# Performance work log

Measured on AMD Instinct MI355X. Metric: run time of the kernel, lower is better.

## Reference

```python
import jax, jax.numpy as jnp
import numpy as np

T, WQ, WS, C, H, W = 2, 75, 25, 640, 10, 10
WAY, SHOT = 5, 5
HID = C // 16
SCALE_VALUE = 30.0
ATTEN_SCALE_VALUE = 50.0
FROM_VALUE = 0.5
VALUE_INTERVAL = 0.3
BN_EPS = 1e-5
NORM_EPS = 1e-12


def _leaky(x):
    return jnp.where(x >= 0, x, 0.2 * x)


def _l2norm(x, axis):
    n = jnp.sqrt(jnp.sum(x * x, axis=axis, keepdims=True))
    return x / jnp.maximum(n, NORM_EPS)


def _embed(x, W_conv, bn_gamma, bn_beta, bn_mean, bn_var):
    # 1x1 conv (no bias) + eval-mode BatchNorm + LeakyReLU(0.2)
    # x: [t, n, c, h, w] -> [t, n, c, h, w]
    y = jnp.einsum('oc,tnchw->tnohw', W_conv, x)
    inv = bn_gamma / jnp.sqrt(bn_var + BN_EPS)
    y = y * inv[:, None, None] + (bn_beta - bn_mean * inv)[:, None, None]
    return _leaky(y)


def setup_inputs() -> dict:
    key = jax.random.key(0)
    ks = jax.random.split(key, 5)
    return {
        'query_feat': jax.random.normal(ks[0], (T, WQ, C, H, W), dtype=jnp.float32),
        'support_feat': jax.random.normal(ks[1], (T, WS, C, H, W), dtype=jnp.float32),
        'W_conv': jax.random.normal(ks[2], (C, C), dtype=jnp.float32) * 0.02,
        'bn_gamma': jnp.ones((C,), jnp.float32),
        'bn_beta': jnp.zeros((C,), jnp.float32),
        'bn_mean': jnp.zeros((C,), jnp.float32),
        'bn_var': jnp.ones((C,), jnp.float32),
        'psi_w1': jax.random.normal(ks[3], (C, HID), dtype=jnp.float32) * 0.04,
        'psi_b1': jnp.zeros((HID,), jnp.float32),
        'psi_w2': jax.random.normal(ks[4], (HID, 1), dtype=jnp.float32) * 0.15,
        'psi_b2': jnp.zeros((1,), jnp.float32),
        'way_num': WAY,
        'shot_num': SHOT,
    }


def reference(query_feat, support_feat, W_conv, bn_gamma, bn_beta, bn_mean, bn_var,
              psi_w1, psi_b1, psi_w2, psi_b2, way_num, shot_num):
    t, wq, c, h, w = query_feat.shape
    ws = support_feat.shape[1]
    hw = h * w

    # embedded + normalized features for the gated branch
    w_query = _embed(query_feat, W_conv, bn_gamma, bn_beta, bn_mean, bn_var)
    w_query = w_query.reshape(t, wq, c, hw).transpose(0, 1, 3, 2)      # [t, wq, hw, c]
    w_support = _embed(support_feat, W_conv, bn_gamma, bn_beta, bn_mean, bn_var)
    w_support = w_support.reshape(t, ws, c, hw).transpose(0, 2, 1, 3).reshape(t, c, ws * hw)
    w_query = _l2norm(w_query, axis=3)
    w_support = _l2norm(w_support, axis=1)

    # cosine similarity of embedded features: [t, wq, hw, ws*hw]
    f_x = jnp.einsum('tqpc,tck->tqpk', w_query, w_support)

    # AEAModule: per-location adaptive threshold from f_psi MLP
    hid = _leaky(w_query @ psi_w1 + psi_b1)                            # [t, wq, hw, HID]
    clamp_value = jax.nn.sigmoid(hid @ psi_w2 + psi_b2) * VALUE_INTERVAL + FROM_VALUE
    clamp_fx = jax.nn.sigmoid(ATTEN_SCALE_VALUE * (f_x - clamp_value))
    atten_score = clamp_fx / jnp.maximum(
        jnp.sum(jnp.abs(clamp_fx), axis=-1, keepdims=True), NORM_EPS)  # L1 normalize

    # raw-feature cosine similarity
    qf = _l2norm(query_feat.reshape(t, wq, c, hw).transpose(0, 1, 3, 2), axis=3)
    sf = _l2norm(support_feat.reshape(t, ws, c, hw).transpose(0, 2, 1, 3).reshape(t, c, ws * hw), axis=1)
    match_score = jnp.einsum('tqpc,tck->tqpk', qf, sf)                 # [t, wq, hw, ws*hw]

    # gate, regroup support axis into (way, shot, hw_s), reduce
    ams = (atten_score * match_score).reshape(t, wq, hw, way_num, shot_num, hw)
    score = ams.sum(axis=-1).mean(axis=(2, 4)) * SCALE_VALUE           # [t, wq, way]
    return score
```

## Files before the change

### kernel.cpp

```cpp
#include <hip/hip_runtime.h>
#include <stdint.h>

#define T_    2
#define WQ_   75
#define WS_   25
#define C_    640
#define HW_   100
#define HID_  40
#define WAY_  5
#define QP_   (WQ_*HW_)
#define SP_   (WS_*HW_)
#define QPAD_ 128
#define KPAD_ 512
#define KROWS_ (WAY_*KPAD_)
#define C8_   (C_/8)
#define BM_   128
#define QSTR_ (C8_*QPAD_*8)

typedef _Float16 f16;
typedef _Float16 f16x8 __attribute__((ext_vector_type(8)));
typedef _Float16 f16x4 __attribute__((ext_vector_type(4)));
typedef _Float16 f16x16 __attribute__((ext_vector_type(16)));
typedef float    f32x4 __attribute__((ext_vector_type(4)));
typedef float    f32x16 __attribute__((ext_vector_type(16)));
typedef uint32_t u32;

__device__ __forceinline__ void gl_lds16(const f16* g, f16* l) {
  __builtin_amdgcn_global_load_lds(
      (const __attribute__((address_space(1))) u32*)g,
      (__attribute__((address_space(3))) u32*)l, 16, 0, 0);
}

__global__ __launch_bounds__(512) void k0_invnorm(
    const float* __restrict__ q, const float* __restrict__ s,
    float* __restrict__ rq_inv, float* __restrict__ rq_nrm,
    float* __restrict__ rs_inv, float* __restrict__ rs_nrm) {
  __shared__ float part[4][128];
  int b = blockIdx.x;
  int t = b / (WQ_ + WS_);
  int n = b % (WQ_ + WS_);
  int tid = threadIdx.x;
  int seg = tid >> 7, p = tid & 127;
  const float* base; float* oi; float* on; int idx;
  if (n < WQ_) {
    base = q + ((size_t)(t*WQ_ + n))*C_*HW_;
    idx = t*QP_ + n*HW_ + p; oi = rq_inv; on = rq_nrm;
  } else {
    int m = n - WQ_;
    base = s + ((size_t)(t*WS_ + m))*C_*HW_;
    idx = t*SP_ + m*HW_ + p; oi = rs_inv; on = rs_nrm;
  }
  float ss = 0.f;
  if (p < HW_) {
    for (int c = seg*160; c < seg*160 + 160; ++c) {
      float v = base[c*HW_ + p]; ss += v*v;
    }
  }
  part[seg][p] = ss;
  __syncthreads();
  if (seg == 0 && p < HW_) {
    float tot = part[0][p] + part[1][p] + part[2][p] + part[3][p];
    float nrm = fmaxf(sqrtf(tot), 1e-12f);
    oi[idx] = 1.f/nrm; on[idx] = nrm;
  }
}

__global__ __launch_bounds__(256) void kw_packW(
    const float* __restrict__ W, const float* __restrict__ w1,
    f16* __restrict__ Wr, f16* __restrict__ Wt8, f16* __restrict__ w1t) {
  int idx = blockIdx.x*256 + threadIdx.x;
  if (idx < C_*C8_) {
    int o = idx / C8_, c8 = idx % C8_;
    f16x8 v;
#pragma unroll
    for (int i = 0; i < 8; ++i) v[i] = (f16)W[(size_t)o*C_ + c8*8 + i];
    *reinterpret_cast<f16x8*>(Wr + (size_t)o*C_ + c8*8) = v;
    *reinterpret_cast<f16x8*>(Wt8 + ((size_t)c8*C_ + o)*8) = v;
  } else if (idx < C_*C8_ + 48*C8_) {
    int k2 = idx - C_*C8_;
    int h = k2 / C8_, c8 = k2 % C8_;
    f16x8 v;
#pragma unroll
    for (int i = 0; i < 8; ++i)
      v[i] = (h < HID_) ? (f16)w1[(size_t)(c8*8+i)*HID_ + h] : (f16)0.f;
    *reinterpret_cast<f16x8*>(w1t + (size_t)h*C_ + c8*8) = v;
  }
}

__global__ __launch_bounds__(256) void k1_pack_qraw(
    const float* __restrict__ q, const float* __restrict__ rq_inv,
    f16* __restrict__ Bq_raw) {
  int b = blockIdx.x;
  int ct = b % 10; b /= 10;
  int qq = b % WQ_; int t = b / WQ_;
  int c0 = ct*64;
  size_t tq = (size_t)t*WQ_ + qq;
  __shared__ float lds[64*HW_];
  const float4* s4 = reinterpret_cast<const float4*>(
      q + ((tq)*C_ + c0)*HW_);
  float4* l4 = reinterpret_cast<float4*>(lds);
  for (int i = threadIdx.x; i < 64*HW_/4; i += 256) l4[i] = s4[i];
  __syncthreads();
  for (int ch = threadIdx.x; ch < 8*QPAD_; ch += 256) {
    int lc8 = ch / QPAD_, p = ch % QPAD_;
    float inv = (p < HW_) ? rq_inv[t*QP_ + qq*HW_ + p] : 0.f;
    f16x8 v;
#pragma unroll
    for (int i = 0; i < 8; ++i) {
      float x = (p < HW_) ? lds[(lc8*8 + i)*HW_ + p] : 0.f;
      v[i] = (f16)(x * inv);
    }
    *reinterpret_cast<f16x8*>(Bq_raw + (tq*C8_ + c0/8 + lc8)*((size_t)QPAD_*8) + (size_t)p*8) = v;
  }
}

__global__ __launch_bounds__(256) void k2_pack_sraw(
    const float* __restrict__ s, const float* __restrict__ rs_inv,
    f16* __restrict__ As_raw) {
  int b = blockIdx.x;
  int ct = b % 10; b /= 10;
  int n = b % WS_; int t = b / WS_;
  int c0 = ct*64;
  __shared__ float lds[64*HW_];
  const float4* s4 = reinterpret_cast<const float4*>(
      s + (((size_t)(t*WS_ + n))*C_ + c0)*HW_);
  float4* l4 = reinterpret_cast<float4*>(lds);
  for (int i = threadIdx.x; i < 64*HW_/4; i += 256) l4[i] = s4[i];
  __syncthreads();
  for (int ch = threadIdx.x; ch < HW_*8; ch += 256) {
    int p = ch / 8, cc = ch % 8;
    float inv = rs_inv[t*SP_ + n*HW_ + p];
    f16x8 v;
#pragma unroll
    for (int i = 0; i < 8; ++i) v[i] = (f16)(lds[(cc*8 + i)*HW_ + p] * inv);
    int k = n*HW_ + p;
    int way = k / 500, ki = k % 500;
    size_t row = (size_t)way*KPAD_ + ki;
    *reinterpret_cast<f16x8*>(As_raw + ((size_t)(t*C8_ + c0/8 + cc)*KROWS_ + row)*8) = v;
  }
}

__global__ __launch_bounds__(512) void k3_embed_support(
    const f16* __restrict__ As_raw, const f16* __restrict__ Wt8,
    const float* __restrict__ rs_nrm,
    const float* __restrict__ g, const float* __restrict__ be,
    const float* __restrict__ mu, const float* __restrict__ va,
    f16* __restrict__ As_emb) {
  int b = blockIdx.x;
  int t = b / (KROWS_/32);
  int row0 = (b % (KROWS_/32)) * 32;
  int tid = threadIdx.x, wv = tid >> 6, lane = tid & 63;
  int mf = wv & 1, nh = wv >> 1;
  __shared__ f16 Alds[32*32];
  __shared__ f16 Blds[32*C_];
  __shared__ float rowss[32];
  f32x4 acc[10];
#pragma unroll
  for (int i = 0; i < 10; ++i) acc[i] = (f32x4){0.f,0.f,0.f,0.f};

  for (int cs = 0; cs < 20; ++cs) {
    if (tid < 128) {
      int c8l = tid >> 5, r = tid & 31;
      *reinterpret_cast<f16x8*>(Alds + (c8l*32 + r)*8) =
        *reinterpret_cast<const f16x8*>(
            As_raw + ((size_t)(t*C8_ + cs*4 + c8l)*KROWS_ + row0 + r)*8);
    }
    const f16x8* bsrc = reinterpret_cast<const f16x8*>(Wt8 + (size_t)(cs*4)*C_*8);
    f16x8* bdst = reinterpret_cast<f16x8*>(Blds);
    for (int i = tid; i < 4*C_; i += 512) bdst[i] = bsrc[i];
    __syncthreads();
    f16x8 a = *reinterpret_cast<const f16x8*>(
        Alds + ((lane>>4)*32 + mf*16 + (lane&15))*8);
#pragma unroll
    for (int nf = 0; nf < 10; ++nf) {
      int o = nh*160 + nf*16 + (lane & 15);
      f16x8 bf = *reinterpret_cast<const f16x8*>(Blds + (((lane>>4)*C_) + o)*8);
      acc[nf] = __builtin_amdgcn_mfma_f32_16x16x32_f16(a, bf, acc[nf], 0, 0, 0);
    }
    __syncthreads();
  }

  if (tid < 32) rowss[tid] = 0.f;
  __syncthreads();
  int rg = lane >> 4, cl = lane & 15;
  int lrow = mf*16 + rg*4;
  int prow = row0 + lrow;
#pragma unroll
  for (int j = 0; j < 4; ++j) {
    int pr = prow + j;
    int way = pr / KPAD_, ki = pr - way*KPAD_;
    bool valid = ki < 500;
    float nrm = valid ? rs_nrm[t*SP_ + way*500 + ki] : 0.f;
    float ssum = 0.f;
#pragma unroll
    for (int nf = 0; nf < 10; ++nf) {
      int o = nh*160 + nf*16 + cl;
      float inv = g[o] / sqrtf(va[o] + 1e-5f);
      float sh = be[o] - mu[o]*inv;
      float y = acc[nf][j]*nrm*inv + sh;
      y = (y >= 0.f) ? y : 0.2f*y;
      if (!valid) y = 0.f;
      acc[nf][j] = y;
      ssum += y*y;
    }
#pragma unroll
    for (int m = 1; m < 16; m <<= 1) ssum += __shfl_xor(ssum, m);
    if (cl == 0) atomicAdd(&rowss[lrow + j], ssum);
  }
  __syncthreads();
#pragma unroll
  for (int j = 0; j < 4; ++j) {
    int pr = prow + j;
    int ki = pr - (pr / KPAD_)*KPAD_;
    if (ki >= 500) continue;
    float invn = 1.f / fmaxf(sqrtf(rowss[lrow + j]), 1e-12f);
#pragma unroll
    for (int nf = 0; nf < 10; ++nf) {
      int o = nh*160 + nf*16 + cl;
      As_emb[((size_t)(t*C8_ + (o>>3))*KROWS_ + pr)*8 + (o&7)] = (f16)(acc[nf][j]*invn);
    }
  }
}

__global__ __launch_bounds__(256, 3) void k4_embed_query(
    const f16* __restrict__ Wr, const f16* __restrict__ Bq_raw,
    const float* __restrict__ rq_nrm,
    const float* __restrict__ g, const float* __restrict__ be,
    const float* __restrict__ mu, const float* __restrict__ va,
    f16* __restrict__ Bq_emb) {
  __shared__ f16 Ab[3][128*32];
  __shared__ f16 Bb[3][4*QPAD_*8];
  int b = blockIdx.x;
  int ot = b % 5; b /= 5;
  int qq = b % WQ_; int t = b / WQ_;
  int o0 = ot*128;
  size_t tq = (size_t)t*WQ_ + qq;
  int tid = threadIdx.x, w = tid >> 6, lane = tid & 63;
  int la_r = lane >> 2, la_c = lane & 3;

  auto stage = [&](int buf, int cs) {
#pragma unroll
    for (int i = 0; i < 2; ++i) {
      int ca = w*2 + i;
      int r = ca*16 + la_r;
      int sc = la_c ^ (r & 3);
      gl_lds16(Wr + (size_t)(o0 + r)*C_ + cs*32 + sc*8, &Ab[buf][ca*512]);
    }
#pragma unroll
    for (int i = 0; i < 2; ++i) {
      int cb = w*2 + i;
      int c8l = cb >> 1;
      size_t src = (tq*C8_ + cs*4 + c8l)*(size_t)(QPAD_*8) + (size_t)((cb&1)*64 + lane)*8;
      gl_lds16(Bq_raw + src, &Bb[buf][(c8l*QPAD_ + (cb&1)*64)*8]);
    }
  };

  f32x4 acc[2][8];
#pragma unroll
  for (int a = 0; a < 2; ++a)
#pragma unroll
    for (int n = 0; n < 8; ++n) acc[a][n] = (f32x4){0.f,0.f,0.f,0.f};

  stage(0, 0);
  stage(1, 1);
  for (int cs = 0; cs < 20; ++cs) {
    int buf = cs % 3;
    if (cs < 19) asm volatile("s_waitcnt vmcnt(4)" ::: "memory");
    else         asm volatile("s_waitcnt vmcnt(0)" ::: "memory");
    __builtin_amdgcn_s_barrier();
    if (cs < 18) stage((cs+2)%3, cs+2);
    __builtin_amdgcn_s_setprio(1);
    f16x8 fa[2];
#pragma unroll
    for (int mi = 0; mi < 2; ++mi) {
      int R = w*32 + mi*16 + (lane & 15);
      int sc = (lane >> 4) ^ (R & 3);
      fa[mi] = *reinterpret_cast<const f16x8*>(&Ab[buf][R*32 + sc*8]);
    }
#pragma unroll
    for (int nf = 0; nf < 8; ++nf) {
      f16x8 fb = *reinterpret_cast<const f16x8*>(
          &Bb[buf][((lane>>4)*QPAD_ + nf*16 + (lane&15))*8]);
#pragma unroll
      for (int mi = 0; mi < 2; ++mi)
        acc[mi][nf] = __builtin_amdgcn_mfma_f32_16x16x32_f16(fa[mi], fb, acc[mi][nf], 0, 0, 0);
    }
    __builtin_amdgcn_s_setprio(0);
  }

#pragma unroll
  for (int mi = 0; mi < 2; ++mi) {
    int obase = o0 + w*32 + mi*16 + (lane>>4)*4;
    float inv4[4], sh4[4];
#pragma unroll
    for (int j = 0; j < 4; ++j) {
      int o = obase + j;
      inv4[j] = g[o] / sqrtf(va[o] + 1e-5f);
      sh4[j] = be[o] - mu[o]*inv4[j];
    }
#pragma unroll
    for (int nf = 0; nf < 8; ++nf) {
      int pp = nf*16 + (lane & 15);
      float nrmv = (pp < HW_) ? rq_nrm[t*QP_ + qq*HW_ + pp] : 0.f;
      f16x4 vv;
#pragma unroll
      for (int j = 0; j < 4; ++j) {
        float y = (pp < HW_) ? (acc[mi][nf][j]*nrmv*inv4[j] + sh4[j]) : 0.f;
        y = (y >= 0.f) ? y : 0.2f*y;
        vv[j] = (f16)y;
      }
      *reinterpret_cast<f16x4*>(
          &Bq_emb[(tq*C8_ + (obase>>3))*((size_t)QPAD_*8) + (size_t)pp*8 + (obase&7)]) = vv;
    }
  }
}

__global__ __launch_bounds__(256) void k5_colnorm_psi(
    const f16* __restrict__ Bq_emb, const f16* __restrict__ w1t,
    const float* __restrict__ b1, const float* __restrict__ w2,
    const float* __restrict__ b2, float* __restrict__ cv,
    float* __restrict__ invq) {
  __shared__ float ssA[2][QPAD_];
  __shared__ float invs[QPAD_];
  __shared__ float hidL[48*QPAD_];
  int bq = blockIdx.x;
  int tid = threadIdx.x, w = tid >> 6, lane = tid & 63;
  size_t base = (size_t)bq * QSTR_;

  {
    int h2 = tid >> 7, pp = tid & 127;
    float ss = 0.f;
    for (int c8 = h2*40; c8 < h2*40 + 40; ++c8) {
      f16x8 v = *reinterpret_cast<const f16x8*>(&Bq_emb[base + ((size_t)c8*QPAD_ + pp)*8]);
#pragma unroll
      for (int i = 0; i < 8; ++i) { float x = (float)v[i]; ss += x*x; }
    }
    ssA[h2][pp] = ss;
  }
  for (int i = tid; i < 48*QPAD_; i += 256) hidL[i] = 0.f;
  __syncthreads();
  if (tid < QPAD_) {
    float ss = ssA[0][tid] + ssA[1][tid];
    float inv = (ss > 0.f) ? (1.f / fmaxf(sqrtf(ss), 1e-12f)) : 0.f;
    invs[tid] = inv;
    invq[bq*QPAD_ + tid] = inv;
  }

  f32x4 acc[3][8];
#pragma unroll
  for (int a = 0; a < 3; ++a)
#pragma unroll
    for (int n = 0; n < 8; ++n) acc[a][n] = (f32x4){0.f,0.f,0.f,0.f};
  for (int r = 0; r < 5; ++r) {
    int cs = w + r*4;
    f16x8 fa[3];
#pragma unroll
    for (int mf = 0; mf < 3; ++mf) {
      int R = mf*16 + (lane & 15);
      fa[mf] = *reinterpret_cast<const f16x8*>(&w1t[(size_t)R*C_ + cs*32 + (lane>>4)*8]);
    }
#pragma unroll
    for (int nf = 0; nf < 8; ++nf) {
      f16x8 fb = *reinterpret_cast<const f16x8*>(
          &Bq_emb[base + ((size_t)(cs*4 + (lane>>4))*QPAD_ + nf*16 + (lane&15))*8]);
#pragma unroll
      for (int mf = 0; mf < 3; ++mf)
        acc[mf][nf] = __builtin_amdgcn_mfma_f32_16x16x32_f16(fa[mf], fb, acc[mf][nf], 0, 0, 0);
    }
  }
  __syncthreads();
  for (int rr = 0; rr < 4; ++rr) {
    if (w == rr) {
#pragma unroll
      for (int mf = 0; mf < 3; ++mf)
#pragma unroll
        for (int nf = 0; nf < 8; ++nf)
#pragma unroll
          for (int j = 0; j < 4; ++j) {
            int row = mf*16 + (lane>>4)*4 + j;
            int col = nf*16 + (lane & 15);
            hidL[row*QPAD_ + col] += acc[mf][nf][j];
          }
    }
    __syncthreads();
  }
  if (tid < QPAD_) {
    float inv = invs[tid];
    float z = b2[0];
    for (int h = 0; h < HID_; ++h) {
      float hv = hidL[h*QPAD_ + tid]*inv + b1[h];
      hv = (hv >= 0.f) ? hv : 0.2f*hv;
      z += hv*w2[h];
    }
    cv[bq*QPAD_ + tid] = 0.3f/(1.f + __expf(-z)) + 0.5f;
  }
}

__global__ __launch_bounds__(256, 3) void k6_main(
    const f16* __restrict__ As_emb, const f16* __restrict__ As_raw,
    const f16* __restrict__ Bq_emb, const f16* __restrict__ Bq_raw,
    const float* __restrict__ cv, const float* __restrict__ invq,
    float* __restrict__ Spart, float* __restrict__ L1part) {
  __shared__ f16 Ab[3][4*BM_*8];
  __shared__ f16 Bb[3][4*QPAD_*8];
  __shared__ float cvs[QPAD_], iqs[QPAD_], Ss[QPAD_], L1s[QPAD_];

  int bid = blockIdx.x;
  int l = (bid & 7)*375 + (bid >> 3);
  int kt = l & 3; int m = l >> 2;
  int q = m % WQ_; int gidx = m / WQ_;
  int t = gidx / WAY_, way = gidx - t*WAY_;

  int tid = threadIdx.x, w = tid >> 6, lane = tid & 63;
  size_t tq = (size_t)t*WQ_ + q;
  if (tid < QPAD_) {
    cvs[tid] = cv[tq*QPAD_ + tid];
    iqs[tid] = invq[tq*QPAD_ + tid];
    Ss[tid] = 0.f; L1s[tid] = 0.f;
  }
  int wrow0 = w*32;
  size_t rowb = (size_t)way*KPAD_ + (size_t)kt*BM_;

  const size_t aoff = ((size_t)(t*C8_ + (w>>1))*KROWS_ + rowb + (w&1)*64 + lane)*8;
  const size_t boff = ((tq*C8_ + (w>>1))*(size_t)QPAD_ + (w&1)*64 + lane)*8;
  const f16* pA = As_raw + aoff;
  const f16* pB = Bq_raw + boff;
  const f16* pA1 = As_emb + aoff;
  const f16* pB1 = Bq_emb + boff;
  const int CS_A = 4*KROWS_*8;
  const int CS_B = 4*QPAD_*8;
  const int A2 = 2*KROWS_*8;
  const int B2 = 2*QPAD_*8;

  auto stage = [&](int buf, const f16* a, const f16* bsrc) {
    gl_lds16(a,      &Ab[buf][w*512]);
    gl_lds16(a + A2, &Ab[buf][(w+4)*512]);
    gl_lds16(bsrc,      &Bb[buf][w*512]);
    gl_lds16(bsrc + B2, &Bb[buf][(w+4)*512]);
  };

  f32x16 acc[4];
  f16x16 mtc[4];
#pragma unroll
  for (int nf = 0; nf < 4; ++nf) acc[nf] = (f32x16)(0.f);
  float Sl[4] = {0,0,0,0}, L1l[4] = {0,0,0,0};

  stage(0, pA, pB); pA += CS_A; pB += CS_B;
  stage(1, pA, pB); pA += CS_A; pB += CS_B;

  for (int ph = 0; ph < 40; ++ph) {
    if (ph == 18) { pA = pA1; pB = pB1; }
    int buf = ph % 3;
    if (ph < 39) asm volatile("s_waitcnt vmcnt(4)" ::: "memory");
    else         asm volatile("s_waitcnt vmcnt(0)" ::: "memory");
    __builtin_amdgcn_s_barrier();
    if (ph < 38) { stage((ph+2)%3, pA, pB); pA += CS_A; pB += CS_B; }
    __builtin_amdgcn_s_setprio(1);
    const f16* Abuf = Ab[buf];
    const f16* Bbuf = Bb[buf];
    int r0 = wrow0 + (lane & 31);
#pragma unroll
    for (int ks = 0; ks < 2; ++ks) {
      int c8l = ks*2 + (lane >> 5);
      f16x8 fa = *reinterpret_cast<const f16x8*>(&Abuf[(c8l*BM_ + r0)*8]);
#pragma unroll
      for (int nf = 0; nf < 4; ++nf) {
        f16x8 fb = *reinterpret_cast<const f16x8*>(
            &Bbuf[(c8l*QPAD_ + nf*32 + (lane & 31))*8]);
        acc[nf] = __builtin_amdgcn_mfma_f32_32x32x16_f16(fa, fb, acc[nf], 0, 0, 0);
      }
    }
    __builtin_amdgcn_s_setprio(0);

    if (ph == 19) {
#pragma unroll
      for (int nf = 0; nf < 4; ++nf)
#pragma unroll
        for (int jj = 0; jj < 16; ++jj) {
          mtc[nf][jj] = (f16)fminf(fmaxf(acc[nf][jj], -8.f), 8.f);
          acc[nf][jj] = 0.f;
        }
    } else if (ph == 39) {
#pragma unroll
      for (int nf = 0; nf < 4; ++nf) {
        int col = nf*32 + (lane & 31);
        float cvv = cvs[col];
        float iq = iqs[col];
#pragma unroll
        for (int jj = 0; jj < 16; ++jj) {
          float fx = acc[nf][jj] * iq;
          float sg = 1.f/(1.f + __expf(-50.f*(fx - cvv)));
          Sl[nf]  += sg * (float)mtc[nf][jj];
          L1l[nf] += sg;
        }
      }
    }
  }

#pragma unroll
  for (int nf = 0; nf < 4; ++nf) {
    float vs = Sl[nf] + __shfl_xor(Sl[nf], 32);
    float vl = L1l[nf] + __shfl_xor(L1l[nf], 32);
    if (lane < 32) {
      atomicAdd(&Ss[nf*32 + lane], vs);
      atomicAdd(&L1s[nf*32 + lane], vl);
    }
  }
  __syncthreads();
  if (tid < QPAD_) {
    size_t o = ((tq*WAY_ + way)*4 + kt)*(size_t)QPAD_ + tid;
    Spart[o] = Ss[tid]; L1part[o] = L1s[tid];
  }
}

__global__ __launch_bounds__(128) void k7_reduce(
    const float* __restrict__ Spart, const float* __restrict__ L1part,
    float* __restrict__ out) {
  int b = blockIdx.x;
  int tid = threadIdx.x;
  __shared__ float red[128];
  float contrib[WAY_] = {0,0,0,0,0};
  if (tid < HW_) {
    size_t base = (size_t)b*WAY_*4*QPAD_;
    float l1 = 0.f;
#pragma unroll
    for (int w = 0; w < WAY_; ++w)
#pragma unroll
      for (int k = 0; k < 4; ++k) l1 += L1part[base + (w*4+k)*QPAD_ + tid];
    l1 = fmaxf(l1, 1e-12f);
#pragma unroll
    for (int w = 0; w < WAY_; ++w) {
      float sv = 0.f;
#pragma unroll
      for (int k = 0; k < 4; ++k) sv += Spart[base + (w*4+k)*QPAD_ + tid];
      contrib[w] = sv / l1;
    }
  }
#pragma unroll
  for (int w = 0; w < WAY_; ++w) {
    red[tid] = contrib[w];
    __syncthreads();
    for (int off = 64; off > 0; off >>= 1) {
      if (tid < off) red[tid] += red[tid + off];
      __syncthreads();
    }
    if (tid == 0) out[b*WAY_ + w] = red[0] * 30.f / (float)(HW_*5);
    __syncthreads();
  }
}

extern "C" void kernel_launch(void* const* d_in, const int* in_sizes, int n_in,
                              void* d_out, int out_size, void* d_ws, size_t ws_size,
                              hipStream_t stream) {
  (void)in_sizes; (void)n_in; (void)out_size; (void)ws_size;
  const float* q  = (const float*)d_in[0];
  const float* s  = (const float*)d_in[1];
  const float* W  = (const float*)d_in[2];
  const float* g  = (const float*)d_in[3];
  const float* be = (const float*)d_in[4];
  const float* mu = (const float*)d_in[5];
  const float* va = (const float*)d_in[6];
  const float* w1 = (const float*)d_in[7];
  const float* b1 = (const float*)d_in[8];
  const float* w2 = (const float*)d_in[9];
  const float* b2 = (const float*)d_in[10];
  float* out = (float*)d_out;
  char* ws = (char*)d_ws;

  size_t off = 0;
  auto nxt = [&](size_t bytes) { size_t o = off; off += (bytes + 255) & ~(size_t)255; return o; };
  float* rq_inv = (float*)(ws + nxt((size_t)T_*QP_*4));
  float* rq_nrm = (float*)(ws + nxt((size_t)T_*QP_*4));
  float* rs_inv = (float*)(ws + nxt((size_t)T_*SP_*4));
  float* rs_nrm = (float*)(ws + nxt((size_t)T_*SP_*4));
  f16* Wr     = (f16*)(ws + nxt((size_t)C_*C_*2));
  f16* Wt8    = (f16*)(ws + nxt((size_t)C_*C_*2));
  f16* w1t    = (f16*)(ws + nxt((size_t)48*C_*2));
  f16* As_raw = (f16*)(ws + nxt((size_t)T_*KROWS_*C_*2));
  f16* As_emb = (f16*)(ws + nxt((size_t)T_*KROWS_*C_*2));
  f16* Bq_raw = (f16*)(ws + nxt((size_t)T_*WQ_*QSTR_*2));
  f16* Bq_emb = (f16*)(ws + nxt((size_t)T_*WQ_*QSTR_*2));
  float* cvp    = (float*)(ws + nxt((size_t)T_*WQ_*QPAD_*4));
  float* invq   = (float*)(ws + nxt((size_t)T_*WQ_*QPAD_*4));
  float* Spart  = (float*)(ws + nxt((size_t)T_*WQ_*WAY_*4*QPAD_*4));
  float* L1part = (float*)(ws + nxt((size_t)T_*WQ_*WAY_*4*QPAD_*4));

  hipMemsetAsync(As_raw, 0, (size_t)T_*KROWS_*C_*2, stream);
  hipMemsetAsync(As_emb, 0, (size_t)T_*KROWS_*C_*2, stream);

  k0_invnorm<<<T_*(WQ_+WS_), 512, 0, stream>>>(q, s, rq_inv, rq_nrm, rs_inv, rs_nrm);
  kw_packW<<<(C_*C8_ + 48*C8_ + 255)/256, 256, 0, stream>>>(W, w1, Wr, Wt8, w1t);
  k1_pack_qraw<<<T_*WQ_*10, 256, 0, stream>>>(q, rq_inv, Bq_raw);
  k2_pack_sraw<<<T_*WS_*10, 256, 0, stream>>>(s, rs_inv, As_raw);
  k3_embed_support<<<T_*(KROWS_/32), 512, 0, stream>>>(As_raw, Wt8, rs_nrm, g, be, mu, va, As_emb);
  k4_embed_query<<<T_*WQ_*5, 256, 0, stream>>>(Wr, Bq_raw, rq_nrm, g, be, mu, va, Bq_emb);
  k5_colnorm_psi<<<T_*WQ_, 256, 0, stream>>>(Bq_emb, w1t, b1, w2, b2, cvp, invq);
  k6_main<<<3000, 256, 0, stream>>>(As_emb, As_raw, Bq_emb, Bq_raw, cvp, invq, Spart, L1part);
  k7_reduce<<<T_*WQ_, 128, 0, stream>>>(Spart, L1part, out);
}
```

Before: 312.2 us.

## Pack query positions densely into 128-wide tiles and enlarge main GEMM M-tile

Query positions are stored contiguously across all queries and cut into 59 tiles of 128, instead of padding each 100-position query up to 128. This removes the wasted padded columns in the embed, psi and main kernels. The main kernel's block tile grows from 128 to 256 support rows, with two MFMA accumulators per warp, and the grid shrinks from 3000 to 1180 blocks with a new XCD mapping. The cost is more registers, an occupancy hint lowered from 3 to 2, and extra memsets to zero the padding of the query buffers.

```diff
diff --git a/kernel.cpp b/kernel.cpp
--- a/kernel.cpp
+++ b/kernel.cpp
@@ -10,12 +10,12 @@
 #define WAY_  5
 #define QP_   (WQ_*HW_)
 #define SP_   (WS_*HW_)
-#define QPAD_ 128
+#define NPT_  59
+#define QT_   (NPT_*128)
 #define KPAD_ 512
 #define KROWS_ (WAY_*KPAD_)
 #define C8_   (C_/8)
-#define BM_   128
-#define QSTR_ (C8_*QPAD_*8)
+#define BM_   256
 
 typedef _Float16 f16;
 typedef _Float16 f16x8 __attribute__((ext_vector_type(8)));
@@ -41,14 +41,14 @@
   int n = b % (WQ_ + WS_);
   int tid = threadIdx.x;
   int seg = tid >> 7, p = tid & 127;
-  const float* base; float* oi; float* on; int idx;
+  const float* base; float* oi; float* on; size_t idx;
   if (n < WQ_) {
     base = q + ((size_t)(t*WQ_ + n))*C_*HW_;
-    idx = t*QP_ + n*HW_ + p; oi = rq_inv; on = rq_nrm;
+    idx = (size_t)t*QT_ + n*HW_ + p; oi = rq_inv; on = rq_nrm;
   } else {
     int m = n - WQ_;
     base = s + ((size_t)(t*WS_ + m))*C_*HW_;
-    idx = t*SP_ + m*HW_ + p; oi = rs_inv; on = rs_nrm;
+    idx = (size_t)t*SP_ + m*HW_ + p; oi = rs_inv; on = rs_nrm;
   }
   float ss = 0.f;
   if (p < HW_) {
@@ -94,23 +94,20 @@
   int ct = b % 10; b /= 10;
   int qq = b % WQ_; int t = b / WQ_;
   int c0 = ct*64;
-  size_t tq = (size_t)t*WQ_ + qq;
   __shared__ float lds[64*HW_];
   const float4* s4 = reinterpret_cast<const float4*>(
-      q + ((tq)*C_ + c0)*HW_);
+      q + (((size_t)(t*WQ_ + qq))*C_ + c0)*HW_);
   float4* l4 = reinterpret_cast<float4*>(lds);
   for (int i = threadIdx.x; i < 64*HW_/4; i += 256) l4[i] = s4[i];
   __syncthreads();
-  for (int ch = threadIdx.x; ch < 8*QPAD_; ch += 256) {
-    int lc8 = ch / QPAD_, p = ch % QPAD_;
-    float inv = (p < HW_) ? rq_inv[t*QP_ + qq*HW_ + p] : 0.f;
+  for (int ch = threadIdx.x; ch < 8*HW_; ch += 256) {
+    int lc8 = ch / HW_, p = ch % HW_;
+    float inv = rq_inv[(size_t)t*QT_ + qq*HW_ + p];
     f16x8 v;
 #pragma unroll
-    for (int i = 0; i < 8; ++i) {
-      float x = (p < HW_) ? lds[(lc8*8 + i)*HW_ + p] : 0.f;
-      v[i] = (f16)(x * inv);
-    }
-    *reinterpret_cast<f16x8*>(Bq_raw + (tq*C8_ + c0/8 + lc8)*((size_t)QPAD_*8) + (size_t)p*8) = v;
+    for (int i = 0; i < 8; ++i) v[i] = (f16)(lds[(lc8*8 + i)*HW_ + p] * inv);
+    *reinterpret_cast<f16x8*>(
+        Bq_raw + ((size_t)(t*C8_ + c0/8 + lc8)*QT_ + qq*HW_ + p)*8) = v;
   }
 }
 
@@ -229,12 +226,11 @@
     const float* __restrict__ mu, const float* __restrict__ va,
     f16* __restrict__ Bq_emb) {
   __shared__ f16 Ab[3][128*32];
-  __shared__ f16 Bb[3][4*QPAD_*8];
+  __shared__ f16 Bb[3][4*128*8];
   int b = blockIdx.x;
-  int ot = b % 5; b /= 5;
-  int qq = b % WQ_; int t = b / WQ_;
+  int ot = b % 5; int m = b / 5;
+  int pt = m % NPT_; int t = m / NPT_;
   int o0 = ot*128;
-  size_t tq = (size_t)t*WQ_ + qq;
   int tid = threadIdx.x, w = tid >> 6, lane = tid & 63;
   int la_r = lane >> 2, la_c = lane & 3;
 
@@ -250,8 +246,8 @@
     for (int i = 0; i < 2; ++i) {
       int cb = w*2 + i;
       int c8l = cb >> 1;
-      size_t src = (tq*C8_ + cs*4 + c8l)*(size_t)(QPAD_*8) + (size_t)((cb&1)*64 + lane)*8;
-      gl_lds16(Bq_raw + src, &Bb[buf][(c8l*QPAD_ + (cb&1)*64)*8]);
+      size_t src = ((size_t)(t*C8_ + cs*4 + c8l)*QT_ + pt*128 + (cb&1)*64 + lane)*8;
+      gl_lds16(Bq_raw + src, &Bb[buf][(c8l*128 + (cb&1)*64)*8]);
     }
   };
 
@@ -280,7 +276,7 @@
 #pragma unroll
     for (int nf = 0; nf < 8; ++nf) {
       f16x8 fb = *reinterpret_cast<const f16x8*>(
-          &Bb[buf][((lane>>4)*QPAD_ + nf*16 + (lane&15))*8]);
+          &Bb[buf][((lane>>4)*128 + nf*16 + (lane&15))*8]);
 #pragma unroll
       for (int mi = 0; mi < 2; ++mi)
         acc[mi][nf] = __builtin_amdgcn_mfma_f32_16x16x32_f16(fa[mi], fb, acc[mi][nf], 0, 0, 0);
@@ -300,17 +296,17 @@
     }
 #pragma unroll
     for (int nf = 0; nf < 8; ++nf) {
-      int pp = nf*16 + (lane & 15);
-      float nrmv = (pp < HW_) ? rq_nrm[t*QP_ + qq*HW_ + pp] : 0.f;
+      size_t gp = (size_t)pt*128 + nf*16 + (lane & 15);
+      float nrmv = rq_nrm[(size_t)t*QT_ + gp];
       f16x4 vv;
 #pragma unroll
       for (int j = 0; j < 4; ++j) {
-        float y = (pp < HW_) ? (acc[mi][nf][j]*nrmv*inv4[j] + sh4[j]) : 0.f;
+        float y = (nrmv > 0.f) ? (acc[mi][nf][j]*nrmv*inv4[j] + sh4[j]) : 0.f;
         y = (y >= 0.f) ? y : 0.2f*y;
         vv[j] = (f16)y;
       }
       *reinterpret_cast<f16x4*>(
-          &Bq_emb[(tq*C8_ + (obase>>3))*((size_t)QPAD_*8) + (size_t)pp*8 + (obase&7)]) = vv;
+          &Bq_emb[((size_t)(t*C8_ + (obase>>3))*QT_ + gp)*8 + (obase&7)]) = vv;
     }
   }
 }
@@ -320,30 +316,35 @@
     const float* __restrict__ b1, const float* __restrict__ w2,
     const float* __restrict__ b2, float* __restrict__ cv,
     float* __restrict__ invq) {
-  __shared__ float ssA[2][QPAD_];
-  __shared__ float invs[QPAD_];
-  __shared__ float hidL[48*QPAD_];
+  __shared__ float ssA[2][128];
+  __shared__ float invs[128];
+  __shared__ float hidL[48*128];
   int bq = blockIdx.x;
+  int pt = bq % NPT_, t = bq / NPT_;
   int tid = threadIdx.x, w = tid >> 6, lane = tid & 63;
-  size_t base = (size_t)bq * QSTR_;
+  size_t pbase = (size_t)pt*128;
+
+  auto bptr = [&](int c8, int pp) -> const f16* {
+    return Bq_emb + ((size_t)(t*C8_ + c8)*QT_ + pbase + pp)*8;
+  };
 
   {
     int h2 = tid >> 7, pp = tid & 127;
     float ss = 0.f;
     for (int c8 = h2*40; c8 < h2*40 + 40; ++c8) {
-      f16x8 v = *reinterpret_cast<const f16x8*>(&Bq_emb[base + ((size_t)c8*QPAD_ + pp)*8]);
+      f16x8 v = *reinterpret_cast<const f16x8*>(bptr(c8, pp));
 #pragma unroll
       for (int i = 0; i < 8; ++i) { float x = (float)v[i]; ss += x*x; }
     }
     ssA[h2][pp] = ss;
   }
-  for (int i = tid; i < 48*QPAD_; i += 256) hidL[i] = 0.f;
-  __syncthreads();
-  if (tid < QPAD_) {
+  for (int i = tid; i < 48*128; i += 256) hidL[i] = 0.f;
+  __syncthreads();
+  if (tid < 128) {
     float ss = ssA[0][tid] + ssA[1][tid];
     float inv = (ss > 0.f) ? (1.f / fmaxf(sqrtf(ss), 1e-12f)) : 0.f;
     invs[tid] = inv;
-    invq[bq*QPAD_ + tid] = inv;
+    invq[(size_t)t*QT_ + pbase + tid] = inv;
   }
 
   f32x4 acc[3][8];
@@ -362,7 +363,7 @@
 #pragma unroll
     for (int nf = 0; nf < 8; ++nf) {
       f16x8 fb = *reinterpret_cast<const f16x8*>(
-          &Bq_emb[base + ((size_t)(cs*4 + (lane>>4))*QPAD_ + nf*16 + (lane&15))*8]);
+          bptr(cs*4 + (lane>>4), nf*16 + (lane&15)));
 #pragma unroll
       for (int mf = 0; mf < 3; ++mf)
         acc[mf][nf] = __builtin_amdgcn_mfma_f32_16x16x32_f16(fa[mf], fb, acc[mf][nf], 0, 0, 0);
@@ -379,70 +380,74 @@
           for (int j = 0; j < 4; ++j) {
             int row = mf*16 + (lane>>4)*4 + j;
             int col = nf*16 + (lane & 15);
-            hidL[row*QPAD_ + col] += acc[mf][nf][j];
+            hidL[row*128 + col] += acc[mf][nf][j];
           }
     }
     __syncthreads();
   }
-  if (tid < QPAD_) {
+  if (tid < 128) {
     float inv = invs[tid];
     float z = b2[0];
     for (int h = 0; h < HID_; ++h) {
-      float hv = hidL[h*QPAD_ + tid]*inv + b1[h];
+      float hv = hidL[h*128 + tid]*inv + b1[h];
       hv = (hv >= 0.f) ? hv : 0.2f*hv;
       z += hv*w2[h];
     }
-    cv[bq*QPAD_ + tid] = 0.3f/(1.f + __expf(-z)) + 0.5f;
-  }
-}
-
-__global__ __launch_bounds__(256, 3) void k6_main(
+    cv[(size_t)t*QT_ + pbase + tid] = 0.3f/(1.f + __expf(-z)) + 0.5f;
+  }
+}
+
+__global__ __launch_bounds__(256, 2) void k6_main(
     const f16* __restrict__ As_emb, const f16* __restrict__ As_raw,
     const f16* __restrict__ Bq_emb, const f16* __restrict__ Bq_raw,
     const float* __restrict__ cv, const float* __restrict__ invq,
     float* __restrict__ Spart, float* __restrict__ L1part) {
   __shared__ f16 Ab[3][4*BM_*8];
-  __shared__ f16 Bb[3][4*QPAD_*8];
-  __shared__ float cvs[QPAD_], iqs[QPAD_], Ss[QPAD_], L1s[QPAD_];
+  __shared__ f16 Bb[3][4*128*8];
+  __shared__ float cvs[128], iqs[128], Ss[128], L1s[128];
 
   int bid = blockIdx.x;
-  int l = (bid & 7)*375 + (bid >> 3);
-  int kt = l & 3; int m = l >> 2;
-  int q = m % WQ_; int gidx = m / WQ_;
-  int t = gidx / WAY_, way = gidx - t*WAY_;
+  int xcd = bid & 7, j0 = bid >> 3;
+  int l = (xcd < 4) ? xcd*148 + j0 : 592 + (xcd-4)*147 + j0;
+  int wk = l % 10; int m = l / 10;
+  int pt = m % NPT_; int t = m / NPT_;
+  int way = wk >> 1, kt = wk & 1;
 
   int tid = threadIdx.x, w = tid >> 6, lane = tid & 63;
-  size_t tq = (size_t)t*WQ_ + q;
-  if (tid < QPAD_) {
-    cvs[tid] = cv[tq*QPAD_ + tid];
-    iqs[tid] = invq[tq*QPAD_ + tid];
+  if (tid < 128) {
+    cvs[tid] = cv[(size_t)t*QT_ + pt*128 + tid];
+    iqs[tid] = invq[(size_t)t*QT_ + pt*128 + tid];
     Ss[tid] = 0.f; L1s[tid] = 0.f;
   }
-  int wrow0 = w*32;
+  int wrow0 = w*64;
   size_t rowb = (size_t)way*KPAD_ + (size_t)kt*BM_;
 
-  const size_t aoff = ((size_t)(t*C8_ + (w>>1))*KROWS_ + rowb + (w&1)*64 + lane)*8;
-  const size_t boff = ((tq*C8_ + (w>>1))*(size_t)QPAD_ + (w&1)*64 + lane)*8;
+  const size_t aoff = ((size_t)(t*C8_ + w)*KROWS_ + rowb + lane)*8;
+  const size_t boff = ((size_t)(t*C8_ + w)*QT_ + pt*128 + lane)*8;
   const f16* pA = As_raw + aoff;
   const f16* pB = Bq_raw + boff;
   const f16* pA1 = As_emb + aoff;
   const f16* pB1 = Bq_emb + boff;
   const int CS_A = 4*KROWS_*8;
-  const int CS_B = 4*QPAD_*8;
-  const int A2 = 2*KROWS_*8;
-  const int B2 = 2*QPAD_*8;
+  const int CS_B = 4*QT_*8;
 
   auto stage = [&](int buf, const f16* a, const f16* bsrc) {
-    gl_lds16(a,      &Ab[buf][w*512]);
-    gl_lds16(a + A2, &Ab[buf][(w+4)*512]);
-    gl_lds16(bsrc,      &Bb[buf][w*512]);
-    gl_lds16(bsrc + B2, &Bb[buf][(w+4)*512]);
+    f16* da = &Ab[buf][(size_t)w*BM_*8];
+    f16* db = &Bb[buf][(size_t)w*128*8];
+    gl_lds16(a,        da);
+    gl_lds16(a + 512,  da + 512);
+    gl_lds16(a + 1024, da + 1024);
+    gl_lds16(a + 1536, da + 1536);
+    gl_lds16(bsrc,       db);
+    gl_lds16(bsrc + 512, db + 512);
   };
 
-  f32x16 acc[4];
-  f16x16 mtc[4];
-#pragma unroll
-  for (int nf = 0; nf < 4; ++nf) acc[nf] = (f32x16)(0.f);
+  f32x16 acc[2][4];
+  f16x16 mtc[2][4];
+#pragma unroll
+  for (int mi = 0; mi < 2; ++mi)
+#pragma unroll
+    for (int nf = 0; nf < 4; ++nf) acc[mi][nf] = (f32x16)(0.f);
   float Sl[4] = {0,0,0,0}, L1l[4] = {0,0,0,0};
 
   stage(0, pA, pB); pA += CS_A; pB += CS_B;
@@ -451,7 +456,7 @@
   for (int ph = 0; ph < 40; ++ph) {
     if (ph == 18) { pA = pA1; pB = pB1; }
     int buf = ph % 3;
-    if (ph < 39) asm volatile("s_waitcnt vmcnt(4)" ::: "memory");
+    if (ph < 39) asm volatile("s_waitcnt vmcnt(6)" ::: "memory");
     else         asm volatile("s_waitcnt vmcnt(0)" ::: "memory");
     __builtin_amdgcn_s_barrier();
     if (ph < 38) { stage((ph+2)%3, pA, pB); pA += CS_A; pB += CS_B; }
@@ -462,24 +467,28 @@
 #pragma unroll
     for (int ks = 0; ks < 2; ++ks) {
       int c8l = ks*2 + (lane >> 5);
-      f16x8 fa = *reinterpret_cast<const f16x8*>(&Abuf[(c8l*BM_ + r0)*8]);
+      f16x8 fa0 = *reinterpret_cast<const f16x8*>(&Abuf[(c8l*BM_ + r0)*8]);
+      f16x8 fa1 = *reinterpret_cast<const f16x8*>(&Abuf[(c8l*BM_ + r0 + 32)*8]);
 #pragma unroll
       for (int nf = 0; nf < 4; ++nf) {
         f16x8 fb = *reinterpret_cast<const f16x8*>(
-            &Bbuf[(c8l*QPAD_ + nf*32 + (lane & 31))*8]);
-        acc[nf] = __builtin_amdgcn_mfma_f32_32x32x16_f16(fa, fb, acc[nf], 0, 0, 0);
+            &Bbuf[(c8l*128 + nf*32 + (lane & 31))*8]);
+        acc[0][nf] = __builtin_amdgcn_mfma_f32_32x32x16_f16(fa0, fb, acc[0][nf], 0, 0, 0);
+        acc[1][nf] = __builtin_amdgcn_mfma_f32_32x32x16_f16(fa1, fb, acc[1][nf], 0, 0, 0);
       }
     }
     __builtin_amdgcn_s_setprio(0);
 
     if (ph == 19) {
 #pragma unroll
-      for (int nf = 0; nf < 4; ++nf)
-#pragma unroll
-        for (int jj = 0; jj < 16; ++jj) {
-          mtc[nf][jj] = (f16)fminf(fmaxf(acc[nf][jj], -8.f), 8.f);
-          acc[nf][jj] = 0.f;
-        }
+      for (int mi = 0; mi < 2; ++mi)
+#pragma unroll
+        for (int nf = 0; nf < 4; ++nf)
+#pragma unroll
+          for (int jj = 0; jj < 16; ++jj) {
+            mtc[mi][nf][jj] = (f16)fminf(fmaxf(acc[mi][nf][jj], -8.f), 8.f);
+            acc[mi][nf][jj] = 0.f;
+          }
     } else if (ph == 39) {
 #pragma unroll
       for (int nf = 0; nf < 4; ++nf) {
@@ -487,12 +496,14 @@
         float cvv = cvs[col];
         float iq = iqs[col];
 #pragma unroll
-        for (int jj = 0; jj < 16; ++jj) {
-          float fx = acc[nf][jj] * iq;
-          float sg = 1.f/(1.f + __expf(-50.f*(fx - cvv)));
-          Sl[nf]  += sg * (float)mtc[nf][jj];
-          L1l[nf] += sg;
-        }
+        for (int mi = 0; mi < 2; ++mi)
+#pragma unroll
+          for (int jj = 0; jj < 16; ++jj) {
+            float fx = acc[mi][nf][jj] * iq;
+            float sg = 1.f/(1.f + __expf(-50.f*(fx - cvv)));
+            Sl[nf]  += sg * (float)mtc[mi][nf][jj];
+            L1l[nf] += sg;
+          }
       }
     }
   }
@@ -507,8 +518,8 @@
     }
   }
   __syncthreads();
-  if (tid < QPAD_) {
-    size_t o = ((tq*WAY_ + way)*4 + kt)*(size_t)QPAD_ + tid;
+  if (tid < 128) {
+    size_t o = ((size_t)((t*WAY_ + way)*2 + kt))*QT_ + (size_t)pt*128 + tid;
     Spart[o] = Ss[tid]; L1part[o] = L1s[tid];
   }
 }
@@ -517,22 +528,25 @@
     const float* __restrict__ Spart, const float* __restrict__ L1part,
     float* __restrict__ out) {
   int b = blockIdx.x;
+  int t = b / WQ_, q = b % WQ_;
   int tid = threadIdx.x;
   __shared__ float red[128];
   float contrib[WAY_] = {0,0,0,0,0};
   if (tid < HW_) {
-    size_t base = (size_t)b*WAY_*4*QPAD_;
+    size_t p = (size_t)t*0 + (size_t)q*HW_ + tid;
     float l1 = 0.f;
 #pragma unroll
     for (int w = 0; w < WAY_; ++w)
 #pragma unroll
-      for (int k = 0; k < 4; ++k) l1 += L1part[base + (w*4+k)*QPAD_ + tid];
+      for (int k = 0; k < 2; ++k)
+        l1 += L1part[((size_t)((t*WAY_ + w)*2 + k))*QT_ + p];
     l1 = fmaxf(l1, 1e-12f);
 #pragma unroll
     for (int w = 0; w < WAY_; ++w) {
       float sv = 0.f;
 #pragma unroll
-      for (int k = 0; k < 4; ++k) sv += Spart[base + (w*4+k)*QPAD_ + tid];
+      for (int k = 0; k < 2; ++k)
+        sv += Spart[((size_t)((t*WAY_ + w)*2 + k))*QT_ + p];
       contrib[w] = sv / l1;
     }
   }
@@ -569,8 +583,8 @@
 
   size_t off = 0;
   auto nxt = [&](size_t bytes) { size_t o = off; off += (bytes + 255) & ~(size_t)255; return o; };
-  float* rq_inv = (float*)(ws + nxt((size_t)T_*QP_*4));
-  float* rq_nrm = (float*)(ws + nxt((size_t)T_*QP_*4));
+  float* rq_inv = (float*)(ws + nxt((size_t)T_*QT_*4));
+  float* rq_nrm = (float*)(ws + nxt((size_t)T_*QT_*4));
   float* rs_inv = (float*)(ws + nxt((size_t)T_*SP_*4));
   float* rs_nrm = (float*)(ws + nxt((size_t)T_*SP_*4));
   f16* Wr     = (f16*)(ws + nxt((size_t)C_*C_*2));
@@ -578,23 +592,26 @@
   f16* w1t    = (f16*)(ws + nxt((size_t)48*C_*2));
   f16* As_raw = (f16*)(ws + nxt((size_t)T_*KROWS_*C_*2));
   f16* As_emb = (f16*)(ws + nxt((size_t)T_*KROWS_*C_*2));
-  f16* Bq_raw = (f16*)(ws + nxt((size_t)T_*WQ_*QSTR_*2));
-  f16* Bq_emb = (f16*)(ws + nxt((size_t)T_*WQ_*QSTR_*2));
-  float* cvp    = (float*)(ws + nxt((size_t)T_*WQ_*QPAD_*4));
-  float* invq   = (float*)(ws + nxt((size_t)T_*WQ_*QPAD_*4));
-  float* Spart  = (float*)(ws + nxt((size_t)T_*WQ_*WAY_*4*QPAD_*4));
-  float* L1part = (float*)(ws + nxt((size_t)T_*WQ_*WAY_*4*QPAD_*4));
+  f16* Bq_raw = (f16*)(ws + nxt((size_t)T_*C8_*QT_*8*2));
+  f16* Bq_emb = (f16*)(ws + nxt((size_t)T_*C8_*QT_*8*2));
+  float* cvp    = (float*)(ws + nxt((size_t)T_*QT_*4));
+  float* invq   = (float*)(ws + nxt((size_t)T_*QT_*4));
+  float* Spart  = (float*)(ws + nxt((size_t)T_*WAY_*2*QT_*4));
+  float* L1part = (float*)(ws + nxt((size_t)T_*WAY_*2*QT_*4));
 
   hipMemsetAsync(As_raw, 0, (size_t)T_*KROWS_*C_*2, stream);
   hipMemsetAsync(As_emb, 0, (size_t)T_*KROWS_*C_*2, stream);
+  hipMemsetAsync(Bq_raw, 0, (size_t)T_*C8_*QT_*8*2, stream);
+  hipMemsetAsync(rq_inv, 0, (size_t)T_*QT_*4, stream);
+  hipMemsetAsync(rq_nrm, 0, (size_t)T_*QT_*4, stream);
 
   k0_invnorm<<<T_*(WQ_+WS_), 512, 0, stream>>>(q, s, rq_inv, rq_nrm, rs_inv, rs_nrm);
   kw_packW<<<(C_*C8_ + 48*C8_ + 255)/256, 256, 0, stream>>>(W, w1, Wr, Wt8, w1t);
   k1_pack_qraw<<<T_*WQ_*10, 256, 0, stream>>>(q, rq_inv, Bq_raw);
   k2_pack_sraw<<<T_*WS_*10, 256, 0, stream>>>(s, rs_inv, As_raw);
   k3_embed_support<<<T_*(KROWS_/32), 512, 0, stream>>>(As_raw, Wt8, rs_nrm, g, be, mu, va, As_emb);
-  k4_embed_query<<<T_*WQ_*5, 256, 0, stream>>>(Wr, Bq_raw, rq_nrm, g, be, mu, va, Bq_emb);
-  k5_colnorm_psi<<<T_*WQ_, 256, 0, stream>>>(Bq_emb, w1t, b1, w2, b2, cvp, invq);
-  k6_main<<<3000, 256, 0, stream>>>(As_emb, As_raw, Bq_emb, Bq_raw, cvp, invq, Spart, L1part);
+  k4_embed_query<<<T_*5*NPT_, 256, 0, stream>>>(Wr, Bq_raw, rq_nrm, g, be, mu, va, Bq_emb);
+  k5_colnorm_psi<<<T_*NPT_, 256, 0, stream>>>(Bq_emb, w1t, b1, w2, b2, cvp, invq);
+  k6_main<<<1180, 256, 0, stream>>>(As_emb, As_raw, Bq_emb, Bq_raw, cvp, invq, Spart, L1part);
   k7_reduce<<<T_*WQ_, 128, 0, stream>>>(Spart, L1part, out);
 }
```

Result: faster. 304.0 us (-2.6%).
